# Optimization experiments

Hardware: AMD Instinct MI355X
Metric: run time of the kernel (lower is better)

Reference implementation:

```python
import jax, jax.numpy as jnp
import numpy as np

# model dims (DeepSeekV2-Lite-like, reduced expert count)
H = 2048      # hidden_dim
NH = 16       # num_heads
NOPE = 128    # qk_nope_head_dim
ROPE = 64     # qk_rope_head_dim (interleaved rotary)
VD = 128      # v_head_dim
QL = 1536     # q_lora_rank
KVL = 512     # kv_lora_rank
E = 8         # num routed experts
TOPK = 2      # num_experts_per_token
MI = 512      # moe_intermediate_dim
SH_I = 2 * MI # num_shared_experts * moe_intermediate_dim
B = 1
S = 2048
T = B * S
EPS = 1e-6
MOE_SCALE = 1.0  # gating_scaling_factor


def setup_inputs() -> dict:
    key = jax.random.key(0)
    ks = jax.random.split(key, 16)
    def w(k, shape):
        return jax.random.normal(k, shape, dtype=jnp.float32) * 0.02
    # interleaved rotary tables: one angle per (even,odd) pair
    half = ROPE // 2
    pos = jnp.arange(S, dtype=jnp.float32)
    inv_freq = 1.0 / (10000.0 ** (jnp.arange(half, dtype=jnp.float32) * 2.0 / ROPE))
    ang = pos[:, None] * inv_freq[None, :]              # [S, half]
    sin = jnp.tile(jnp.sin(ang), (B, 1))                # [T, half]
    cos = jnp.tile(jnp.cos(ang), (B, 1))
    return {
        "x": jax.random.normal(ks[0], (T, H), jnp.float32),
        "skip": jax.random.normal(ks[1], (T, H), jnp.float32),
        "rotary_sin": sin,
        "rotary_cos": cos,
        "ln1_w": jnp.ones((H,), jnp.float32),
        "ln2_w": jnp.ones((H,), jnp.float32),
        "w_qa": w(ks[2], (QL, H)),
        "qa_norm_w": jnp.ones((QL,), jnp.float32),
        "w_qb": w(ks[3], (NH * (NOPE + ROPE), QL)),
        "w_kva": w(ks[4], (KVL + ROPE, H)),
        "kva_norm_w": jnp.ones((KVL,), jnp.float32),
        "w_kb": w(ks[5], (NH * NOPE, KVL)),
        "w_vb": w(ks[6], (NH * VD, KVL)),
        "w_o": w(ks[7], (H, NH * VD)),
        "gate_w": w(ks[8], (E, H)),
        "moe_up_w": w(ks[9], (E, 2 * MI, H)),
        "moe_down_w": w(ks[10], (E, H, MI)),
        "shared_up_w": w(ks[11], (2 * SH_I, H)),
        "shared_down_w": w(ks[12], (H, SH_I)),
        "batch": B,
    }


def _rms(v, w):
    return v * jax.lax.rsqrt(jnp.mean(v * v, axis=-1, keepdims=True) + EPS) * w


def _rope_interleaved(v, sin, cos):
    # v: [T, nh, ROPE]; sin/cos: [T, ROPE//2]; rotate (even, odd) pairs
    x1, x2 = v[..., 0::2], v[..., 1::2]
    s, c = sin[:, None, :], cos[:, None, :]
    o1 = x1 * c - x2 * s
    o2 = x1 * s + x2 * c
    return jnp.stack([o1, o2], axis=-1).reshape(v.shape)


def reference(x, skip, rotary_sin, rotary_cos, ln1_w, ln2_w, w_qa, qa_norm_w,
              w_qb, w_kva, kva_norm_w, w_kb, w_vb, w_o, gate_w,
              moe_up_w, moe_down_w, shared_up_w, shared_down_w, batch):
    Tt = x.shape[0]
    Sq = Tt // batch
    # SkipRMSNorm #1
    x1 = x + skip
    n1 = _rms(x1, ln1_w)
    # ---- MLA attention (prefill path, decoding_batches=0) ----
    qa = _rms(n1 @ w_qa.T, qa_norm_w)                               # [T, QL]
    q = (qa @ w_qb.T).reshape(Tt, NH, NOPE + ROPE)
    q_nope, q_pe = q[..., :NOPE], q[..., NOPE:]
    q_pe = _rope_interleaved(q_pe, rotary_sin, rotary_cos)
    kv = n1 @ w_kva.T                                               # [T, KVL+ROPE]
    ckv = _rms(kv[:, :KVL], kva_norm_w)
    k_pe = _rope_interleaved(kv[:, KVL:][:, None, :], rotary_sin, rotary_cos)  # [T,1,ROPE]
    k_nope = (ckv @ w_kb.T).reshape(Tt, NH, NOPE)
    v = (ckv @ w_vb.T).reshape(Tt, NH, VD)
    qf = jnp.concatenate([q_nope, q_pe], -1).reshape(batch, Sq, NH, NOPE + ROPE)
    kf = jnp.concatenate([k_nope, jnp.broadcast_to(k_pe, (Tt, NH, ROPE))], -1)
    kf = kf.reshape(batch, Sq, NH, NOPE + ROPE)
    vf = v.reshape(batch, Sq, NH, VD)
    scale = 1.0 / np.sqrt(NOPE + ROPE)
    scores = jnp.einsum('bqhd,bkhd->bhqk', qf, kf) * scale
    causal = jnp.tril(jnp.ones((Sq, Sq), bool))
    scores = jnp.where(causal[None, None], scores, jnp.float32(-1e30))
    p = jax.nn.softmax(scores, axis=-1)
    o = jnp.einsum('bhqk,bkhd->bqhd', p, vf).reshape(Tt, NH * VD)
    attn = o @ w_o.T
    # SkipRMSNorm #2
    x2 = x1 + attn
    n2 = _rms(x2, ln2_w)
    # ---- MoE FFN: softmax gate, greedy top-k, normalized probs ----
    probs = jax.nn.softmax(n2 @ gate_w.T, axis=-1)                  # [T, E]
    tv, ti = jax.lax.top_k(probs, TOPK)
    tv = tv / jnp.sum(tv, axis=-1, keepdims=True) * MOE_SCALE
    routed = jnp.zeros_like(n2)
    for e in range(E):  # fixed small expert count; masked dense dispatch
        we = jnp.sum(tv * (ti == e), axis=-1)                       # [T]
        h = n2 @ moe_up_w[e].T                                      # [T, 2*MI]
        h = jax.nn.silu(h[:, :MI]) * h[:, MI:]
        routed = routed + we[:, None] * (h @ moe_down_w[e].T)
    # shared experts (dense swiglu MLP)
    hs = n2 @ shared_up_w.T
    hs = jax.nn.silu(hs[:, :SH_I]) * hs[:, SH_I:]
    ffn = routed + hs @ shared_down_w.T
    return (x2, ffn)
```

## Files before the change

### kernel.cpp

```cpp
#include <hip/hip_runtime.h>
#include <hip/hip_bf16.h>

#define H 2048
#define NH 16
#define NOPE 128
#define ROPE_D 64
#define DQK 192
#define VD 128
#define QL 1536
#define KVL 512
#define NE 8
#define MI_D 512
#define SHI 1024
#define EPS 1e-6f
#define MAXA 5120

typedef unsigned short bfu;
typedef short bf16x8 __attribute__((ext_vector_type(8)));
typedef float f32x4 __attribute__((ext_vector_type(4)));

#define MFMA16(a, b, c) __builtin_amdgcn_mfma_f32_16x16x32_bf16(a, b, c, 0, 0, 0)

__device__ __forceinline__ float bf2f(bfu u) {
    union { unsigned int i; float f; } w; w.i = ((unsigned int)u) << 16; return w.f;
}
__device__ __forceinline__ bfu f2bf(float f) {
    union { float f; unsigned int i; } u; u.f = f;
    return (bfu)((u.i + 0x7fffu + ((u.i >> 16) & 1u)) >> 16);
}

__device__ __forceinline__ void async16(const bfu* g, bfu* l) {
    __builtin_amdgcn_global_load_lds((const __attribute__((address_space(1))) void*)g,
                                     (__attribute__((address_space(3))) void*)l, 16, 0, 0);
}

__device__ __forceinline__ float blk_sum(float v) {
    __shared__ float sb[4];
    for (int o = 32; o > 0; o >>= 1) v += __shfl_down(v, o, 64);
    int lane = threadIdx.x & 63, w = threadIdx.x >> 6;
    __syncthreads();
    if (lane == 0) sb[w] = v;
    __syncthreads();
    return sb[0] + sb[1] + sb[2] + sb[3];
}

template<int MODE>
__global__ __launch_bounds__(256) void gemm_mfma(const bfu* __restrict__ A, const bfu* __restrict__ B,
                                                 void* __restrict__ Cv, void* __restrict__ Cv2,
                                                 int M, int N, int K, int ldm3,
                                                 const int* __restrict__ aidx,
                                                 const int* __restrict__ eid, long bstride) {
    __shared__ bfu sA[2][128 * 32];
    __shared__ bfu sB[2][128 * 32];
    const int tid = threadIdx.x;
    const int lane = tid & 63, w = tid >> 6;
    const int quad = lane >> 4, li = lane & 15;
    const int m0 = blockIdx.y * 128, n0 = blockIdx.x * 128;
    const bfu* Bp = B + (eid ? (size_t)eid[blockIdx.y] * bstride : 0);

    const int l4 = lane >> 2;
    const int lg = lane & 3;
    const int kc = lg ^ ((lane >> 3) & 3);
    int r0 = m0 + w * 32 + l4, r1 = r0 + 16;
    if (aidx) { r0 = aidx[r0]; r1 = aidx[r1]; }
    const bfu* gA0 = A + (size_t)r0 * K + kc * 8;
    const bfu* gA1 = A + (size_t)r1 * K + kc * 8;
    const bfu* gB0 = Bp + (size_t)(n0 + w * 32 + l4) * K + kc * 8;
    const bfu* gB1 = gB0 + (size_t)16 * K;
    const int oA0 = (w * 32) * 32, oA1 = (w * 32 + 16) * 32;

    const int wm = (w >> 1) * 64, wn = (w & 1) * 64;
    const int fg = (quad ^ ((li >> 1) & 3)) * 8;
    int oa[4], ob[4];
#pragma unroll
    for (int t4 = 0; t4 < 4; ++t4) {
        oa[t4] = (wm + t4 * 16 + li) * 32 + fg;
        ob[t4] = (wn + t4 * 16 + li) * 32 + fg;
    }
    f32x4 acc[4][4];
#pragma unroll
    for (int i = 0; i < 4; ++i)
#pragma unroll
        for (int j = 0; j < 4; ++j) acc[i][j] = (f32x4){0.f, 0.f, 0.f, 0.f};

    const int nb = K / 32;
    async16(gA0, &sA[0][oA0]); async16(gA1, &sA[0][oA1]);
    async16(gB0, &sB[0][oA0]); async16(gB1, &sB[0][oA1]);

    for (int it = 0; it < nb; ++it) {
        const int cur = it & 1;
        __syncthreads();
        bf16x8 av[4], bv[4];
#pragma unroll
        for (int t4 = 0; t4 < 4; ++t4) av[t4] = *(const bf16x8*)&sA[cur][oa[t4]];
#pragma unroll
        for (int t4 = 0; t4 < 4; ++t4) bv[t4] = *(const bf16x8*)&sB[cur][ob[t4]];
        if (it + 1 < nb) {
            const int k1 = (it + 1) * 32, nxt = cur ^ 1;
            async16(gA0 + k1, &sA[nxt][oA0]); async16(gA1 + k1, &sA[nxt][oA1]);
            async16(gB0 + k1, &sB[nxt][oA0]); async16(gB1 + k1, &sB[nxt][oA1]);
        }
#pragma unroll
        for (int mt = 0; mt < 4; ++mt)
#pragma unroll
            for (int nt = 0; nt < 4; ++nt)
                acc[mt][nt] = MFMA16(av[mt], bv[nt], acc[mt][nt]);
    }

#pragma unroll
    for (int mt = 0; mt < 4; ++mt)
#pragma unroll
        for (int nt = 0; nt < 4; ++nt) {
            int row = m0 + wm + mt * 16 + quad * 4;
            int col = n0 + wn + nt * 16 + li;
            if (MODE == 0) {
                float* C = (float*)Cv;
#pragma unroll
                for (int r = 0; r < 4; ++r) C[(size_t)(row + r) * N + col] = acc[mt][nt][r];
            } else if (MODE == 1) {
                bfu* C = (bfu*)Cv;
#pragma unroll
                for (int r = 0; r < 4; ++r) C[(size_t)(row + r) * N + col] = f2bf(acc[mt][nt][r]);
            } else {
                if (n0 < 2048) {
                    bfu* C = (bfu*)Cv;
#pragma unroll
                    for (int r = 0; r < 4; ++r) C[(size_t)(row + r) * 2048 + col] = f2bf(acc[mt][nt][r]);
                } else {
                    bfu* C2 = (bfu*)Cv2;
                    ushort4 u;
                    u.x = f2bf(acc[mt][nt][0]); u.y = f2bf(acc[mt][nt][1]);
                    u.z = f2bf(acc[mt][nt][2]); u.w = f2bf(acc[mt][nt][3]);
                    *(ushort4*)(C2 + (size_t)(col - 2048) * ldm3 + row) = u;
                }
            }
        }
}

__global__ __launch_bounds__(256) void k_cast(const float* __restrict__ s, bfu* __restrict__ d) {
    size_t i = ((size_t)blockIdx.x * 256 + threadIdx.x) * 8;
    float4 a = *(const float4*)(s + i);
    float4 b = *(const float4*)(s + i + 4);
    ushort4 u0, u1;
    u0.x = f2bf(a.x); u0.y = f2bf(a.y); u0.z = f2bf(a.z); u0.w = f2bf(a.w);
    u1.x = f2bf(b.x); u1.y = f2bf(b.y); u1.z = f2bf(b.z); u1.w = f2bf(b.w);
    *(ushort4*)(d + i) = u0;
    *(ushort4*)(d + i + 4) = u1;
}

__global__ __launch_bounds__(256) void k_cast_kva(const float* __restrict__ s, bfu* __restrict__ d) {
    size_t i = ((size_t)blockIdx.x * 256 + threadIdx.x) * 8;
    int row = (int)(i >> 11);
    ushort4 u0 = {0, 0, 0, 0}, u1 = {0, 0, 0, 0};
    if (row < 576) {
        float4 a = *(const float4*)(s + i);
        float4 b = *(const float4*)(s + i + 4);
        u0.x = f2bf(a.x); u0.y = f2bf(a.y); u0.z = f2bf(a.z); u0.w = f2bf(a.w);
        u1.x = f2bf(b.x); u1.y = f2bf(b.y); u1.z = f2bf(b.z); u1.w = f2bf(b.w);
    }
    *(ushort4*)(d + i) = u0;
    *(ushort4*)(d + i + 4) = u1;
}

__global__ __launch_bounds__(256) void k_add_rms(const float* __restrict__ x, const float* __restrict__ skip,
                                                 const float* __restrict__ w,
                                                 float* __restrict__ x1, bfu* __restrict__ n1b) {
    int t = blockIdx.x;
    size_t base = (size_t)t * H;
    float loc[8]; float ss = 0.f;
#pragma unroll
    for (int i = 0; i < 8; ++i) {
        int c = threadIdx.x + i * 256;
        float v = x[base + c] + skip[base + c];
        loc[i] = v; ss += v * v;
        x1[base + c] = v;
    }
    float tot = blk_sum(ss);
    float r = rsqrtf(tot / (float)H + EPS);
#pragma unroll
    for (int i = 0; i < 8; ++i) {
        int c = threadIdx.x + i * 256;
        n1b[base + c] = f2bf(loc[i] * r * w[c]);
    }
}

__global__ __launch_bounds__(256) void k_rms_bf(const bfu* __restrict__ src, const float* __restrict__ w,
                                                bfu* __restrict__ dst, int len, int sstr) {
    int t = blockIdx.x;
    const bfu* row = src + (size_t)t * sstr;
    int n = len / 256;
    float loc[6]; float ss = 0.f;
    for (int i = 0; i < n; ++i) { float v = bf2f(row[threadIdx.x + i * 256]); loc[i] = v; ss += v * v; }
    float tot = blk_sum(ss);
    float r = rsqrtf(tot / (float)len + EPS);
    for (int i = 0; i < n; ++i) {
        int c = threadIdx.x + i * 256;
        dst[(size_t)t * len + c] = f2bf(loc[i] * r * w[c]);
    }
}

__global__ __launch_bounds__(256) void k_kv_post(const bfu* __restrict__ qkv, const float* __restrict__ kw,
                                                 const float* __restrict__ sin_, const float* __restrict__ cos_,
                                                 bfu* __restrict__ ckv, bfu* __restrict__ kpe) {
    int t = blockIdx.x;
    const bfu* row = qkv + (size_t)t * 2176 + 1536;
    float v0 = bf2f(row[threadIdx.x]), v1 = bf2f(row[threadIdx.x + 256]);
    float tot = blk_sum(v0 * v0 + v1 * v1);
    float r = rsqrtf(tot / 512.f + EPS);
    ckv[(size_t)t * 512 + threadIdx.x]       = f2bf(v0 * r * kw[threadIdx.x]);
    ckv[(size_t)t * 512 + threadIdx.x + 256] = f2bf(v1 * r * kw[threadIdx.x + 256]);
    if (threadIdx.x < 32) {
        int p = threadIdx.x;
        float x1v = bf2f(row[512 + 2 * p]), x2v = bf2f(row[512 + 2 * p + 1]);
        float s = sin_[t * 32 + p], c = cos_[t * 32 + p];
        kpe[(size_t)t * 64 + 2 * p]     = f2bf(x1v * c - x2v * s);
        kpe[(size_t)t * 64 + 2 * p + 1] = f2bf(x1v * s + x2v * c);
    }
}

__global__ __launch_bounds__(256) void k_flash_mfma(const bfu* __restrict__ qb,
                                                    const bfu* __restrict__ kn,
                                                    const bfu* __restrict__ kpe,
                                                    const bfu* __restrict__ vt,
                                                    bfu* __restrict__ O,
                                                    const float* __restrict__ rsin,
                                                    const float* __restrict__ rcos, int T) {
    __shared__ bfu Ks[32 * 200];
    __shared__ bfu VtL[128 * 32];
    __shared__ bfu P[64 * 40];
    const int tid = threadIdx.x;
    const int lane = tid & 63, w = tid >> 6;
    const int quad = lane >> 4, li = lane & 15;
    const int q0 = ((int)gridDim.x - 1 - (int)blockIdx.x) * 64;
    const int h = blockIdx.y;
    const float scale = 0.07216878364870322f;

    bf16x8 qf[6];
    {
        int qrow = q0 + w * 16 + li;
        const bfu* qp = qb + ((size_t)qrow * NH + h) * DQK;
#pragma unroll
        for (int s6 = 0; s6 < 6; ++s6) {
            bf16x8 v = *(const bf16x8*)(qp + s6 * 32 + quad * 8);
            if (s6 >= 4) {
                int pb = (s6 - 4) * 16 + quad * 4;
#pragma unroll
                for (int j = 0; j < 4; ++j) {
                    float x1 = bf2f((bfu)v[2 * j]), x2 = bf2f((bfu)v[2 * j + 1]);
                    float s = rsin[qrow * 32 + pb + j], c = rcos[qrow * 32 + pb + j];
                    v[2 * j]     = (short)f2bf(x1 * c - x2 * s);
                    v[2 * j + 1] = (short)f2bf(x1 * s + x2 * c);
                }
            }
            qf[s6] = v;
        }
    }
    f32x4 accO[8];
#pragma unroll
    for (int i = 0; i < 8; ++i) accO[i] = (f32x4){0.f, 0.f, 0.f, 0.f};
    float lrow[4] = {0.f, 0.f, 0.f, 0.f};

    int kr[3], kg[3];
#pragma unroll
    for (int it = 0; it < 3; ++it) { int G = tid + it * 256; kr[it] = G / 24; kg[it] = G % 24; }
    int vn[2], vgl[2], vkc[2];
#pragma unroll
    for (int it = 0; it < 2; ++it) {
        int idx = tid + it * 256; vn[it] = idx >> 2; vgl[it] = idx & 3;
        vkc[it] = vgl[it] ^ ((vn[it] >> 1) & 3);
    }
    bf16x8 kreg[3], vreg[2];
#pragma unroll
    for (int it = 0; it < 3; ++it)
        kreg[it] = (kg[it] < 16) ? *(const bf16x8*)(kn + (size_t)kr[it] * (NH * 128) + h * 128 + kg[it] * 8)
                                 : *(const bf16x8*)(kpe + (size_t)kr[it] * 64 + (kg[it] - 16) * 8);
#pragma unroll
    for (int it = 0; it < 2; ++it)
        vreg[it] = *(const bf16x8*)(vt + (size_t)(h * 128 + vn[it]) * T + vkc[it] * 8);

    const int fgv = (quad ^ ((li >> 1) & 3)) * 8;
    const int kend = q0 + 64;
    for (int k0 = 0; k0 < kend; k0 += 32) {
        __syncthreads();
#pragma unroll
        for (int it = 0; it < 3; ++it) *(bf16x8*)(Ks + kr[it] * 200 + kg[it] * 8) = kreg[it];
#pragma unroll
        for (int it = 0; it < 2; ++it) *(bf16x8*)(VtL + vn[it] * 32 + vgl[it] * 8) = vreg[it];
        if (k0 + 32 < kend) {
            int k1 = k0 + 32;
#pragma unroll
            for (int it = 0; it < 3; ++it)
                kreg[it] = (kg[it] < 16) ? *(const bf16x8*)(kn + (size_t)(k1 + kr[it]) * (NH * 128) + h * 128 + kg[it] * 8)
                                         : *(const bf16x8*)(kpe + (size_t)(k1 + kr[it]) * 64 + (kg[it] - 16) * 8);
#pragma unroll
            for (int it = 0; it < 2; ++it)
                vreg[it] = *(const bf16x8*)(vt + (size_t)(h * 128 + vn[it]) * T + k1 + vkc[it] * 8);
        }
        __syncthreads();
        f32x4 s[2];
#pragma unroll
        for (int ct = 0; ct < 2; ++ct) {
            f32x4 a = (f32x4){0.f, 0.f, 0.f, 0.f};
#pragma unroll
            for (int s6 = 0; s6 < 6; ++s6) {
                bf16x8 kf = *(const bf16x8*)(Ks + (ct * 16 + li) * 200 + s6 * 32 + quad * 8);
                a = MFMA16(qf[s6], kf, a);
            }
            s[ct] = a;
        }
#pragma unroll
        for (int r = 0; r < 4; ++r) {
            int row = q0 + w * 16 + quad * 4 + r;
            float p0 = (k0 + li <= row) ? __expf(s[0][r] * scale) : 0.f;
            float p1 = (k0 + 16 + li <= row) ? __expf(s[1][r] * scale) : 0.f;
            s[0][r] = p0; s[1][r] = p1;
            lrow[r] += p0 + p1;
        }
#pragma unroll
        for (int ct = 0; ct < 2; ++ct)
#pragma unroll
            for (int r = 0; r < 4; ++r)
                P[(w * 16 + quad * 4 + r) * 40 + ct * 16 + li] = f2bf(s[ct][r]);
        bf16x8 pf = *(const bf16x8*)(P + (w * 16 + li) * 40 + quad * 8);
#pragma unroll
        for (int v8 = 0; v8 < 8; ++v8) {
            bf16x8 vf = *(const bf16x8*)(VtL + (v8 * 16 + li) * 32 + fgv);
            accO[v8] = MFMA16(pf, vf, accO[v8]);
        }
    }
#pragma unroll
    for (int r = 0; r < 4; ++r) {
        float l = lrow[r];
        l += __shfl_xor(l, 1); l += __shfl_xor(l, 2);
        l += __shfl_xor(l, 4); l += __shfl_xor(l, 8);
        lrow[r] = 1.0f / l;
    }
#pragma unroll
    for (int v8 = 0; v8 < 8; ++v8)
#pragma unroll
        for (int r = 0; r < 4; ++r) {
            float val = accO[v8][r] * lrow[r];
            O[(size_t)(q0 + w * 16 + quad * 4 + r) * (NH * 128) + h * 128 + v8 * 16 + li] = f2bf(val);
        }
}

__global__ __launch_bounds__(256) void k_x2_n2(const float* __restrict__ x1, const bfu* __restrict__ attn,
                                               const float* __restrict__ ln2w, float* __restrict__ outx2,
                                               bfu* __restrict__ n2b, const float* __restrict__ gw,
                                               int* __restrict__ eidx, float* __restrict__ wts,
                                               int* __restrict__ cnt) {
    int t = blockIdx.x;
    size_t base = (size_t)t * H;
    float loc[8]; float ss = 0.f;
#pragma unroll
    for (int i = 0; i < 8; ++i) {
        int c = threadIdx.x + i * 256;
        float vv = x1[base + c] + bf2f(attn[base + c]);
        loc[i] = vv; ss += vv * vv;
        outx2[base + c] = vv;
    }
    float tot = blk_sum(ss);
    float r = rsqrtf(tot / (float)H + EPS);
    float pe[NE] = {0.f, 0.f, 0.f, 0.f, 0.f, 0.f, 0.f, 0.f};
#pragma unroll
    for (int i = 0; i < 8; ++i) {
        int c = threadIdx.x + i * 256;
        float nv = loc[i] * r * ln2w[c];
        n2b[base + c] = f2bf(nv);
#pragma unroll
        for (int e = 0; e < NE; ++e) pe[e] += nv * gw[e * H + c];
    }
    __shared__ float logits[NE];
    for (int e = 0; e < NE; ++e) {
        float tt = blk_sum(pe[e]);
        if (threadIdx.x == 0) logits[e] = tt;
    }
    __syncthreads();
    if (threadIdx.x == 0) {
        float m = logits[0];
        for (int e = 1; e < NE; ++e) m = fmaxf(m, logits[e]);
        float p[NE];
        for (int e = 0; e < NE; ++e) p[e] = __expf(logits[e] - m);
        int i1 = 0;
        for (int e = 1; e < NE; ++e) if (p[e] > p[i1]) i1 = e;
        int i2 = -1;
        for (int e = 0; e < NE; ++e) if (e != i1 && (i2 < 0 || p[e] > p[i2])) i2 = e;
        float denom = p[i1] + p[i2];
        eidx[t * 2] = i1; eidx[t * 2 + 1] = i2;
        wts[t * 2] = p[i1] / denom; wts[t * 2 + 1] = p[i2] / denom;
        atomicAdd(&cnt[i1], 1); atomicAdd(&cnt[i2], 1);
    }
}

__global__ __launch_bounds__(256) void k_moe_init(int* __restrict__ cnt, int* __restrict__ slot,
                                                  int* __restrict__ eid, int* __restrict__ idx,
                                                  float* __restrict__ aw) {
    int tid = threadIdx.x;
    if (tid < NE) { cnt[tid] = 0; slot[tid] = 0; }
    if (tid < 40) eid[tid] = 0;
    for (int i = tid; i < MAXA; i += 256) { idx[i] = 0; aw[i] = 0.f; }
}

__global__ __launch_bounds__(64) void k_moe_scan(const int* __restrict__ cnt, int* __restrict__ base,
                                                 int* __restrict__ eid) {
    if (threadIdx.x == 0) {
        int off = 0;
        for (int e = 0; e < NE; ++e) {
            base[e] = off;
            int nb = (cnt[e] + 127) >> 7;
            for (int j = 0; j < nb; ++j) eid[(off >> 7) + j] = e;
            off += nb << 7;
        }
    }
}

__global__ __launch_bounds__(256) void k_moe_scatter(const int* __restrict__ eidx, const float* __restrict__ wts,
                                                     const int* __restrict__ base, int* __restrict__ slot,
                                                     int* __restrict__ idx, float* __restrict__ aw,
                                                     int* __restrict__ posmap) {
    int t = blockIdx.x * 256 + threadIdx.x;
#pragma unroll
    for (int j = 0; j < 2; ++j) {
        int e = eidx[t * 2 + j];
        int p = base[e] + atomicAdd(&slot[e], 1);
        idx[p] = t; aw[p] = wts[t * 2 + j]; posmap[t * 2 + j] = p;
    }
}

__global__ __launch_bounds__(256) void k_silu_sparse(const bfu* __restrict__ hb, const float* __restrict__ aw,
                                                     bfu* __restrict__ g) {
    int row = blockIdx.x;
    float we = aw[row];
    const bfu* hr = hb + (size_t)row * 1024;
    bfu* gr = g + (size_t)row * 512;
#pragma unroll
    for (int j = 0; j < 2; ++j) {
        int i = threadIdx.x + j * 256;
        float a = bf2f(hr[i]), b = bf2f(hr[512 + i]);
        gr[i] = f2bf(we * a / (1.0f + __expf(-a)) * b);
    }
}

__global__ __launch_bounds__(256) void k_silu_sh(const bfu* __restrict__ hb, bfu* __restrict__ g) {
    int t = blockIdx.x;
    const bfu* row = hb + (size_t)t * 2048;
    bfu* grow = g + (size_t)t * 1024;
#pragma unroll
    for (int j = 0; j < 4; ++j) {
        int i = threadIdx.x + j * 256;
        float a = bf2f(row[i]), b = bf2f(row[1024 + i]);
        grow[i] = f2bf(a / (1.0f + __expf(-a)) * b);
    }
}

__global__ __launch_bounds__(256) void k_ffn_out(const float* __restrict__ routed, const bfu* __restrict__ dsp,
                                                 const int* __restrict__ posmap, float* __restrict__ out,
                                                 size_t TH) {
    int t = blockIdx.x;
    int p1 = posmap[t * 2], p2 = posmap[t * 2 + 1];
    const bfu* d1 = dsp + (size_t)p1 * H;
    const bfu* d2 = dsp + (size_t)p2 * H;
#pragma unroll
    for (int j = 0; j < 8; ++j) {
        int c = threadIdx.x + j * 256;
        out[TH + (size_t)t * H + c] = routed[(size_t)t * H + c] + bf2f(d1[c]) + bf2f(d2[c]);
    }
}

extern "C" void kernel_launch(void* const* d_in, const int* in_sizes, int n_in,
                              void* d_out, int out_size, void* d_ws, size_t ws_size,
                              hipStream_t stream) {
    const float* x      = (const float*)d_in[0];
    const float* skip   = (const float*)d_in[1];
    const float* rsin   = (const float*)d_in[2];
    const float* rcos   = (const float*)d_in[3];
    const float* ln1w   = (const float*)d_in[4];
    const float* ln2w   = (const float*)d_in[5];
    const float* w_qa   = (const float*)d_in[6];
    const float* qa_nw  = (const float*)d_in[7];
    const float* w_qb   = (const float*)d_in[8];
    const float* w_kva  = (const float*)d_in[9];
    const float* kva_nw = (const float*)d_in[10];
    const float* w_kb   = (const float*)d_in[11];
    const float* w_vb   = (const float*)d_in[12];
    const float* w_o    = (const float*)d_in[13];
    const float* gate_w = (const float*)d_in[14];
    const float* mup    = (const float*)d_in[15];
    const float* mdown  = (const float*)d_in[16];
    const float* shup   = (const float*)d_in[17];
    const float* shdown = (const float*)d_in[18];

    const int T = in_sizes[0] / H;

    bfu* WB = (bfu*)d_ws;
    bfu* wqkv_b  = WB + 0;
    bfu* wkbv_b  = WB + 4456448;
    bfu* wqb_b   = WB + 6553600;
    bfu* wo_b    = WB + 11272192;
    bfu* mup_b   = WB + 15466496;
    bfu* mdown_b = WB + 32243712;
    bfu* shup_b  = WB + 40632320;
    bfu* shdn_b  = WB + 44826624;
    const size_t WBYTES = 93847552;

    char* AB = (char*)d_ws + WBYTES;
    float* x1f    = (float*)(AB + 0);
    float* routed = (float*)(AB + 0);
    bfu*   n1b    = (bfu*)(AB + 16777216);
    bfu*   qkvb   = (bfu*)(AB + 25165824);
    bfu*   knb    = (bfu*)(AB + 25165824);
    bfu*   hsp    = (bfu*)(AB + 25165824);
    bfu*   qab    = (bfu*)(AB + 35651584);
    bfu*   gsp    = (bfu*)(AB + 35651584);
    bfu*   qbb    = (bfu*)(AB + 41943040);
    bfu*   attnb  = (bfu*)(AB + 41943040);
    bfu*   ckvb   = (bfu*)(AB + 54525952);
    bfu*   kpeb   = (bfu*)(AB + 56623104);
    char*  G      = AB + 56885248;
    int*   eidx   = (int*)(G);
    float* wts    = (float*)(G + 16384);
    int*   posmap = (int*)(G + 32768);
    int*   midx   = (int*)(G + 49152);
    float* maw    = (float*)(G + 69632);
    int*   mcnt   = (int*)(G + 90112);
    int*   mbase  = (int*)(G + 90112 + 64);
    int*   mslot  = (int*)(G + 90112 + 128);
    int*   meid   = (int*)(G + 90112 + 192);
    bfu*   ob     = (bfu*)(AB + 57016320);
    bfu*   gsb    = (bfu*)(AB + 57016320);
    bfu*   vtb    = (bfu*)(AB + 65404928);
    bfu*   hsb    = (bfu*)(AB + 65404928);
    bfu*   dsp    = (bfu*)(AB + 65404928);
    const size_t REQ = WBYTES + 86376448;
    if (ws_size < REQ) return;

    k_cast<<<1536, 256, 0, stream>>>(w_qa, wqkv_b);
    k_cast_kva<<<640, 256, 0, stream>>>(w_kva, wqkv_b + 3145728);
    k_cast<<<512, 256, 0, stream>>>(w_kb, wkbv_b);
    k_cast<<<512, 256, 0, stream>>>(w_vb, wkbv_b + 1048576);
    k_cast<<<2304, 256, 0, stream>>>(w_qb, wqb_b);
    k_cast<<<2048, 256, 0, stream>>>(w_o, wo_b);
    k_cast<<<8192, 256, 0, stream>>>(mup, mup_b);
    k_cast<<<4096, 256, 0, stream>>>(mdown, mdown_b);
    k_cast<<<2048, 256, 0, stream>>>(shup, shup_b);
    k_cast<<<1024, 256, 0, stream>>>(shdown, shdn_b);

    k_add_rms<<<T, 256, 0, stream>>>(x, skip, ln1w, x1f, n1b);
    gemm_mfma<1><<<dim3(2176 / 128, T / 128), 256, 0, stream>>>(n1b, wqkv_b, qkvb, nullptr, T, 2176, H, 0, nullptr, nullptr, 0);
    k_rms_bf<<<T, 256, 0, stream>>>(qkvb, qa_nw, qab, QL, 2176);
    k_kv_post<<<T, 256, 0, stream>>>(qkvb, kva_nw, rsin, rcos, ckvb, kpeb);
    gemm_mfma<1><<<dim3((NH * DQK) / 128, T / 128), 256, 0, stream>>>(qab, wqb_b, qbb, nullptr, T, NH * DQK, QL, 0, nullptr, nullptr, 0);
    gemm_mfma<4><<<dim3(4096 / 128, T / 128), 256, 0, stream>>>(ckvb, wkbv_b, knb, vtb, T, 4096, KVL, T, nullptr, nullptr, 0);
    k_flash_mfma<<<dim3(T / 64, NH), 256, 0, stream>>>(qbb, knb, kpeb, vtb, ob, rsin, rcos, T);
    gemm_mfma<1><<<dim3(H / 128, T / 128), 256, 0, stream>>>(ob, wo_b, attnb, nullptr, T, H, NH * VD, 0, nullptr, nullptr, 0);
    k_moe_init<<<1, 256, 0, stream>>>(mcnt, mslot, meid, midx, maw);
    k_x2_n2<<<T, 256, 0, stream>>>(x1f, attnb, ln2w, (float*)d_out, n1b, gate_w, eidx, wts, mcnt);
    k_moe_scan<<<1, 64, 0, stream>>>(mcnt, mbase, meid);
    k_moe_scatter<<<T / 256, 256, 0, stream>>>(eidx, wts, mbase, mslot, midx, maw, posmap);
    gemm_mfma<1><<<dim3(2048 / 128, T / 128), 256, 0, stream>>>(n1b, shup_b, hsb, nullptr, T, 2048, H, 0, nullptr, nullptr, 0);
    k_silu_sh<<<T, 256, 0, stream>>>(hsb, gsb);
    gemm_mfma<0><<<dim3(H / 128, T / 128), 256, 0, stream>>>(gsb, shdn_b, routed, nullptr, T, H, SHI, 0, nullptr, nullptr, 0);
    gemm_mfma<1><<<dim3(1024 / 128, MAXA / 128), 256, 0, stream>>>(
        n1b, mup_b, hsp, nullptr, MAXA, 1024, H, 0, midx, meid, (long)1024 * H);
    k_silu_sparse<<<MAXA, 256, 0, stream>>>(hsp, maw, gsp);
    gemm_mfma<1><<<dim3(H / 128, MAXA / 128), 256, 0, stream>>>(
        gsp, mdown_b, dsp, nullptr, MAXA, H, MI_D, 0, nullptr, meid, (long)H * MI_D);
    k_ffn_out<<<T, 256, 0, stream>>>(routed, dsp, posmap, (float*)d_out, (size_t)T * H);
}
```

Before: 697.6 us.

## Triple-buffer GEMM loads, fuse cast and norm kernels, shrink flash tiles

```diff
diff --git a/kernel.cpp b/kernel.cpp
--- a/kernel.cpp
+++ b/kernel.cpp
@@ -21,6 +21,11 @@
 
 #define MFMA16(a, b, c) __builtin_amdgcn_mfma_f32_16x16x32_bf16(a, b, c, 0, 0, 0)
 
+#define BAR_PLAIN()   asm volatile("s_barrier" ::: "memory")
+#define BAR_LGKM0()   asm volatile("s_waitcnt lgkmcnt(0)\n\ts_barrier" ::: "memory")
+#define BAR_VM4()     asm volatile("s_waitcnt vmcnt(4)\n\ts_barrier" ::: "memory")
+#define BAR_VM0()     asm volatile("s_waitcnt vmcnt(0)\n\ts_barrier" ::: "memory")
+
 __device__ __forceinline__ float bf2f(bfu u) {
     union { unsigned int i; float f; } w; w.i = ((unsigned int)u) << 16; return w.f;
 }
@@ -50,8 +55,8 @@
                                                  int M, int N, int K, int ldm3,
                                                  const int* __restrict__ aidx,
                                                  const int* __restrict__ eid, long bstride) {
-    __shared__ bfu sA[2][128 * 32];
-    __shared__ bfu sB[2][128 * 32];
+    __shared__ bfu sA[3][128 * 32];
+    __shared__ bfu sB[3][128 * 32];
     const int tid = threadIdx.x;
     const int lane = tid & 63, w = tid >> 6;
     const int quad = lane >> 4, li = lane & 15;
@@ -86,17 +91,20 @@
     const int nb = K / 32;
     async16(gA0, &sA[0][oA0]); async16(gA1, &sA[0][oA1]);
     async16(gB0, &sB[0][oA0]); async16(gB1, &sB[0][oA1]);
-
+    async16(gA0 + 32, &sA[1][oA0]); async16(gA1 + 32, &sA[1][oA1]);
+    async16(gB0 + 32, &sB[1][oA0]); async16(gB1 + 32, &sB[1][oA1]);
+
+    int cur = 0;
     for (int it = 0; it < nb; ++it) {
-        const int cur = it & 1;
-        __syncthreads();
+        if (it < nb - 1) { BAR_VM4(); } else { BAR_VM0(); }
         bf16x8 av[4], bv[4];
 #pragma unroll
         for (int t4 = 0; t4 < 4; ++t4) av[t4] = *(const bf16x8*)&sA[cur][oa[t4]];
 #pragma unroll
         for (int t4 = 0; t4 < 4; ++t4) bv[t4] = *(const bf16x8*)&sB[cur][ob[t4]];
-        if (it + 1 < nb) {
-            const int k1 = (it + 1) * 32, nxt = cur ^ 1;
+        if (it + 2 < nb) {
+            const int k1 = (it + 2) * 32;
+            int nxt = cur + 2; if (nxt >= 3) nxt -= 3;
             async16(gA0 + k1, &sA[nxt][oA0]); async16(gA1 + k1, &sA[nxt][oA1]);
             async16(gB0 + k1, &sB[nxt][oA0]); async16(gB1 + k1, &sB[nxt][oA1]);
         }
@@ -105,6 +113,7 @@
 #pragma unroll
             for (int nt = 0; nt < 4; ++nt)
                 acc[mt][nt] = MFMA16(av[mt], bv[nt], acc[mt][nt]);
+        if (++cur >= 3) cur = 0;
     }
 
 #pragma unroll
@@ -137,29 +146,30 @@
         }
 }
 
-__global__ __launch_bounds__(256) void k_cast(const float* __restrict__ s, bfu* __restrict__ d) {
-    size_t i = ((size_t)blockIdx.x * 256 + threadIdx.x) * 8;
-    float4 a = *(const float4*)(s + i);
-    float4 b = *(const float4*)(s + i + 4);
-    ushort4 u0, u1;
-    u0.x = f2bf(a.x); u0.y = f2bf(a.y); u0.z = f2bf(a.z); u0.w = f2bf(a.w);
-    u1.x = f2bf(b.x); u1.y = f2bf(b.y); u1.z = f2bf(b.z); u1.w = f2bf(b.w);
-    *(ushort4*)(d + i) = u0;
-    *(ushort4*)(d + i + 4) = u1;
-}
-
-__global__ __launch_bounds__(256) void k_cast_kva(const float* __restrict__ s, bfu* __restrict__ d) {
-    size_t i = ((size_t)blockIdx.x * 256 + threadIdx.x) * 8;
-    int row = (int)(i >> 11);
+struct CastArgs {
+    const float* s[10];
+    bfu* d[10];
+    unsigned start[11];
+    int pad[10];
+};
+__global__ __launch_bounds__(256) void k_cast_all(CastArgs a) {
+    unsigned g = blockIdx.x * 256 + threadIdx.x;
+    if (g >= a.start[10]) return;
+    int id = 0;
+#pragma unroll
+    for (int i = 1; i < 10; ++i) if (g >= a.start[i]) id = i;
+    size_t i8 = (size_t)(g - a.start[id]) * 8;
     ushort4 u0 = {0, 0, 0, 0}, u1 = {0, 0, 0, 0};
-    if (row < 576) {
-        float4 a = *(const float4*)(s + i);
-        float4 b = *(const float4*)(s + i + 4);
-        u0.x = f2bf(a.x); u0.y = f2bf(a.y); u0.z = f2bf(a.z); u0.w = f2bf(a.w);
-        u1.x = f2bf(b.x); u1.y = f2bf(b.y); u1.z = f2bf(b.z); u1.w = f2bf(b.w);
-    }
-    *(ushort4*)(d + i) = u0;
-    *(ushort4*)(d + i + 4) = u1;
+    if (!a.pad[id] || (i8 >> 11) < 576) {
+        const float* s = a.s[id];
+        float4 x0 = *(const float4*)(s + i8);
+        float4 x1 = *(const float4*)(s + i8 + 4);
+        u0.x = f2bf(x0.x); u0.y = f2bf(x0.y); u0.z = f2bf(x0.z); u0.w = f2bf(x0.w);
+        u1.x = f2bf(x1.x); u1.y = f2bf(x1.y); u1.z = f2bf(x1.z); u1.w = f2bf(x1.w);
+    }
+    bfu* d = a.d[id];
+    *(ushort4*)(d + i8) = u0;
+    *(ushort4*)(d + i8 + 4) = u1;
 }
 
 __global__ __launch_bounds__(256) void k_add_rms(const float* __restrict__ x, const float* __restrict__ skip,
@@ -184,41 +194,41 @@
     }
 }
 
-__global__ __launch_bounds__(256) void k_rms_bf(const bfu* __restrict__ src, const float* __restrict__ w,
-                                                bfu* __restrict__ dst, int len, int sstr) {
+__global__ __launch_bounds__(256) void k_qkv_post(const bfu* __restrict__ qkv,
+                                                  const float* __restrict__ qa_nw,
+                                                  const float* __restrict__ kva_nw,
+                                                  const float* __restrict__ sin_, const float* __restrict__ cos_,
+                                                  bfu* __restrict__ qab, bfu* __restrict__ ckv,
+                                                  bfu* __restrict__ kpe) {
     int t = blockIdx.x;
-    const bfu* row = src + (size_t)t * sstr;
-    int n = len / 256;
-    float loc[6]; float ss = 0.f;
-    for (int i = 0; i < n; ++i) { float v = bf2f(row[threadIdx.x + i * 256]); loc[i] = v; ss += v * v; }
-    float tot = blk_sum(ss);
-    float r = rsqrtf(tot / (float)len + EPS);
-    for (int i = 0; i < n; ++i) {
+    const bfu* row = qkv + (size_t)t * 2176;
+    float qa[6]; float ss1 = 0.f;
+#pragma unroll
+    for (int i = 0; i < 6; ++i) {
+        float v = bf2f(row[threadIdx.x + i * 256]); qa[i] = v; ss1 += v * v;
+    }
+    float v0 = bf2f(row[1536 + threadIdx.x]), v1 = bf2f(row[1792 + threadIdx.x]);
+    float s1 = blk_sum(ss1);
+    float s2 = blk_sum(v0 * v0 + v1 * v1);
+    float r1 = rsqrtf(s1 / (float)QL + EPS);
+    float r2 = rsqrtf(s2 / 512.f + EPS);
+#pragma unroll
+    for (int i = 0; i < 6; ++i) {
         int c = threadIdx.x + i * 256;
-        dst[(size_t)t * len + c] = f2bf(loc[i] * r * w[c]);
-    }
-}
-
-__global__ __launch_bounds__(256) void k_kv_post(const bfu* __restrict__ qkv, const float* __restrict__ kw,
-                                                 const float* __restrict__ sin_, const float* __restrict__ cos_,
-                                                 bfu* __restrict__ ckv, bfu* __restrict__ kpe) {
-    int t = blockIdx.x;
-    const bfu* row = qkv + (size_t)t * 2176 + 1536;
-    float v0 = bf2f(row[threadIdx.x]), v1 = bf2f(row[threadIdx.x + 256]);
-    float tot = blk_sum(v0 * v0 + v1 * v1);
-    float r = rsqrtf(tot / 512.f + EPS);
-    ckv[(size_t)t * 512 + threadIdx.x]       = f2bf(v0 * r * kw[threadIdx.x]);
-    ckv[(size_t)t * 512 + threadIdx.x + 256] = f2bf(v1 * r * kw[threadIdx.x + 256]);
+        qab[(size_t)t * QL + c] = f2bf(qa[i] * r1 * qa_nw[c]);
+    }
+    ckv[(size_t)t * 512 + threadIdx.x]       = f2bf(v0 * r2 * kva_nw[threadIdx.x]);
+    ckv[(size_t)t * 512 + threadIdx.x + 256] = f2bf(v1 * r2 * kva_nw[threadIdx.x + 256]);
     if (threadIdx.x < 32) {
         int p = threadIdx.x;
-        float x1v = bf2f(row[512 + 2 * p]), x2v = bf2f(row[512 + 2 * p + 1]);
+        float x1v = bf2f(row[2048 + 2 * p]), x2v = bf2f(row[2048 + 2 * p + 1]);
         float s = sin_[t * 32 + p], c = cos_[t * 32 + p];
         kpe[(size_t)t * 64 + 2 * p]     = f2bf(x1v * c - x2v * s);
         kpe[(size_t)t * 64 + 2 * p + 1] = f2bf(x1v * s + x2v * c);
     }
 }
 
-__global__ __launch_bounds__(256) void k_flash_mfma(const bfu* __restrict__ qb,
+__global__ __launch_bounds__(128) void k_flash_mfma(const bfu* __restrict__ qb,
                                                     const bfu* __restrict__ kn,
                                                     const bfu* __restrict__ kpe,
                                                     const bfu* __restrict__ vt,
@@ -227,11 +237,11 @@
                                                     const float* __restrict__ rcos, int T) {
     __shared__ bfu Ks[32 * 200];
     __shared__ bfu VtL[128 * 32];
-    __shared__ bfu P[64 * 40];
+    __shared__ bfu P[32 * 40];
     const int tid = threadIdx.x;
     const int lane = tid & 63, w = tid >> 6;
     const int quad = lane >> 4, li = lane & 15;
-    const int q0 = ((int)gridDim.x - 1 - (int)blockIdx.x) * 64;
+    const int q0 = ((int)gridDim.x - 1 - (int)blockIdx.x) * 32;
     const int h = blockIdx.y;
     const float scale = 0.07216878364870322f;
 
@@ -260,43 +270,43 @@
     for (int i = 0; i < 8; ++i) accO[i] = (f32x4){0.f, 0.f, 0.f, 0.f};
     float lrow[4] = {0.f, 0.f, 0.f, 0.f};
 
-    int kr[3], kg[3];
-#pragma unroll
-    for (int it = 0; it < 3; ++it) { int G = tid + it * 256; kr[it] = G / 24; kg[it] = G % 24; }
-    int vn[2], vgl[2], vkc[2];
-#pragma unroll
-    for (int it = 0; it < 2; ++it) {
-        int idx = tid + it * 256; vn[it] = idx >> 2; vgl[it] = idx & 3;
+    int kr[6], kg[6];
+#pragma unroll
+    for (int it = 0; it < 6; ++it) { int G = tid + it * 128; kr[it] = G / 24; kg[it] = G % 24; }
+    int vn[4], vgl[4], vkc[4];
+#pragma unroll
+    for (int it = 0; it < 4; ++it) {
+        int idx = tid + it * 128; vn[it] = idx >> 2; vgl[it] = idx & 3;
         vkc[it] = vgl[it] ^ ((vn[it] >> 1) & 3);
     }
-    bf16x8 kreg[3], vreg[2];
-#pragma unroll
-    for (int it = 0; it < 3; ++it)
+    bf16x8 kreg[6], vreg[4];
+#pragma unroll
+    for (int it = 0; it < 6; ++it)
         kreg[it] = (kg[it] < 16) ? *(const bf16x8*)(kn + (size_t)kr[it] * (NH * 128) + h * 128 + kg[it] * 8)
                                  : *(const bf16x8*)(kpe + (size_t)kr[it] * 64 + (kg[it] - 16) * 8);
 #pragma unroll
-    for (int it = 0; it < 2; ++it)
+    for (int it = 0; it < 4; ++it)
         vreg[it] = *(const bf16x8*)(vt + (size_t)(h * 128 + vn[it]) * T + vkc[it] * 8);
 
     const int fgv = (quad ^ ((li >> 1) & 3)) * 8;
-    const int kend = q0 + 64;
+    const int kend = q0 + 32;
     for (int k0 = 0; k0 < kend; k0 += 32) {
-        __syncthreads();
-#pragma unroll
-        for (int it = 0; it < 3; ++it) *(bf16x8*)(Ks + kr[it] * 200 + kg[it] * 8) = kreg[it];
-#pragma unroll
-        for (int it = 0; it < 2; ++it) *(bf16x8*)(VtL + vn[it] * 32 + vgl[it] * 8) = vreg[it];
+        BAR_PLAIN();
+#pragma unroll
+        for (int it = 0; it < 6; ++it) *(bf16x8*)(Ks + kr[it] * 200 + kg[it] * 8) = kreg[it];
+#pragma unroll
+        for (int it = 0; it < 4; ++it) *(bf16x8*)(VtL + vn[it] * 32 + vgl[it] * 8) = vreg[it];
         if (k0 + 32 < kend) {
             int k1 = k0 + 32;
 #pragma unroll
-            for (int it = 0; it < 3; ++it)
+            for (int it = 0; it < 6; ++it)
                 kreg[it] = (kg[it] < 16) ? *(const bf16x8*)(kn + (size_t)(k1 + kr[it]) * (NH * 128) + h * 128 + kg[it] * 8)
                                          : *(const bf16x8*)(kpe + (size_t)(k1 + kr[it]) * 64 + (kg[it] - 16) * 8);
 #pragma unroll
-            for (int it = 0; it < 2; ++it)
+            for (int it = 0; it < 4; ++it)
                 vreg[it] = *(const bf16x8*)(vt + (size_t)(h * 128 + vn[it]) * T + k1 + vkc[it] * 8);
         }
-        __syncthreads();
+        BAR_LGKM0();
         f32x4 s[2];
 #pragma unroll
         for (int ct = 0; ct < 2; ++ct) {
@@ -534,24 +544,24 @@
     const size_t REQ = WBYTES + 86376448;
     if (ws_size < REQ) return;
 
-    k_cast<<<1536, 256, 0, stream>>>(w_qa, wqkv_b);
-    k_cast_kva<<<640, 256, 0, stream>>>(w_kva, wqkv_b + 3145728);
-    k_cast<<<512, 256, 0, stream>>>(w_kb, wkbv_b);
-    k_cast<<<512, 256, 0, stream>>>(w_vb, wkbv_b + 1048576);
-    k_cast<<<2304, 256, 0, stream>>>(w_qb, wqb_b);
-    k_cast<<<2048, 256, 0, stream>>>(w_o, wo_b);
-    k_cast<<<8192, 256, 0, stream>>>(mup, mup_b);
-    k_cast<<<4096, 256, 0, stream>>>(mdown, mdown_b);
-    k_cast<<<2048, 256, 0, stream>>>(shup, shup_b);
-    k_cast<<<1024, 256, 0, stream>>>(shdown, shdn_b);
+    {
+        CastArgs ca;
+        const float* ss[10] = {w_qa, w_kva, w_kb, w_vb, w_qb, w_o, mup, mdown, shup, shdown};
+        bfu* dd[10] = {wqkv_b, wqkv_b + 3145728, wkbv_b, wkbv_b + 1048576, wqb_b,
+                       wo_b, mup_b, mdown_b, shup_b, shdn_b};
+        unsigned n8[10] = {393216, 163840, 131072, 131072, 589824, 524288, 2097152, 1048576, 524288, 262144};
+        unsigned acc = 0;
+        for (int i = 0; i < 10; ++i) { ca.s[i] = ss[i]; ca.d[i] = dd[i]; ca.start[i] = acc; acc += n8[i]; ca.pad[i] = (i == 1); }
+        ca.start[10] = acc;
+        k_cast_all<<<22912, 256, 0, stream>>>(ca);
+    }
 
     k_add_rms<<<T, 256, 0, stream>>>(x, skip, ln1w, x1f, n1b);
     gemm_mfma<1><<<dim3(2176 / 128, T / 128), 256, 0, stream>>>(n1b, wqkv_b, qkvb, nullptr, T, 2176, H, 0, nullptr, nullptr, 0);
-    k_rms_bf<<<T, 256, 0, stream>>>(qkvb, qa_nw, qab, QL, 2176);
-    k_kv_post<<<T, 256, 0, stream>>>(qkvb, kva_nw, rsin, rcos, ckvb, kpeb);
+    k_qkv_post<<<T, 256, 0, stream>>>(qkvb, qa_nw, kva_nw, rsin, rcos, qab, ckvb, kpeb);
     gemm_mfma<1><<<dim3((NH * DQK) / 128, T / 128), 256, 0, stream>>>(qab, wqb_b, qbb, nullptr, T, NH * DQK, QL, 0, nullptr, nullptr, 0);
     gemm_mfma<4><<<dim3(4096 / 128, T / 128), 256, 0, stream>>>(ckvb, wkbv_b, knb, vtb, T, 4096, KVL, T, nullptr, nullptr, 0);
-    k_flash_mfma<<<dim3(T / 64, NH), 256, 0, stream>>>(qbb, knb, kpeb, vtb, ob, rsin, rcos, T);
+    k_flash_mfma<<<dim3(T / 32, NH), 128, 0, stream>>>(qbb, knb, kpeb, vtb, ob, rsin, rcos, T);
     gemm_mfma<1><<<dim3(H / 128, T / 128), 256, 0, stream>>>(ob, wo_b, attnb, nullptr, T, H, NH * VD, 0, nullptr, nullptr, 0);
     k_moe_init<<<1, 256, 0, stream>>>(mcnt, mslot, meid, midx, maw);
     k_x2_n2<<<T, 256, 0, stream>>>(x1f, attnb, ln2w, (float*)d_out, n1b, gate_w, eidx, wts, mcnt);
```

Measured after the change: 678.6 us. -2.7%, faster.
